# Kernel optimization log

Measured on AMD Instinct MI355X. Metric: run time of the kernel, lower is better.

## Reference

```python
import jax, jax.numpy as jnp
import numpy as np

R_MAX = 5.0
NUM_BESSEL = 8
P_CUT = 5.0
AVG_NEIGH = 16.0
SQ3 = 1.7320508075688772


def poly_cutoff(r):
    # PolynomialCutoff with p=5
    u = r / R_MAX
    p = P_CUT
    f = 1.0 - (p + 1.0) * (p + 2.0) / 2.0 * u**5 + p * (p + 2.0) * u**6 - p * (p + 1.0) / 2.0 * u**7
    return f * (u < 1.0)


def bessel_damped(r, t):
    # BesselSinBasis with heat-kernel diffusion damping exp(-k_n^2 t)
    n = jnp.arange(1, NUM_BESSEL + 1, dtype=r.dtype)  # [8]
    k = n * jnp.pi / R_MAX
    pref = jnp.sqrt(2.0 / R_MAX)
    return pref * jnp.sin(k * r) / r * jnp.exp(-(k**2) * t)  # [E,8]


def switch_norm(x, w, b, mw, vw, rm, rv, eps=1e-5):
    # SwitchNorm1d, eval mode (BN stats = running buffers)
    mean_ln = x.mean(1, keepdims=True)
    var_ln = x.var(1, keepdims=True, ddof=1)
    mws = jax.nn.softmax(mw)
    vws = jax.nn.softmax(vw)
    mean = mws[0] * mean_ln + mws[1] * rm
    var = vws[0] * var_ln + vws[1] * rv
    return (x - mean) / jnp.sqrt(var + eps) * w + b


def setup_inputs() -> dict:
    key = jax.random.key(0)
    ks = jax.random.split(key, 16)
    N, E = 10000, 160000
    d = {}
    d["node_feats"] = jax.random.normal(ks[0], (N, 512), jnp.float32)
    d["edge_attrs"] = jax.random.normal(ks[1], (E, 4), jnp.float32)
    d["edge_lengths"] = jax.random.uniform(ks[2], (E, 1), jnp.float32, 0.5, 4.9)
    d["t"] = jax.random.uniform(ks[3], (E, 1), jnp.float32, 0.01, 1.0)
    d["lengths"] = d["edge_lengths"]
    d["edge_index"] = jax.random.randint(ks[4], (2, E), 0, N)
    g = lambda k, sh: jax.random.normal(k, sh, jnp.float32)
    d["W_scalar"] = g(ks[5], (128, 128))
    d["W_up0"] = g(ks[6], (128, 128))
    d["W_up1"] = g(ks[7], (128, 128))
    d["sn_weight"] = jnp.ones((1, 265), jnp.float32)
    d["sn_bias"] = jnp.zeros((1, 265), jnp.float32)
    d["sn_mean_w"] = jnp.ones((2,), jnp.float32)
    d["sn_var_w"] = jnp.ones((2,), jnp.float32)
    d["sn_run_mean"] = jnp.zeros((1, 265), jnp.float32)
    d["sn_run_var"] = jnp.zeros((1, 265), jnp.float32)
    d["W1"] = g(ks[8], (265, 64))
    d["W2"] = g(ks[9], (64, 64))
    d["W3"] = g(ks[10], (64, 64))
    d["W4"] = g(ks[11], (64, 512))
    d["W_out0"] = g(ks[12], (256, 128))
    d["W_out1"] = g(ks[13], (256, 128))
    return d


def reference(node_feats, edge_attrs, edge_lengths, t, lengths, edge_index,
              W_scalar, W_up0, W_up1,
              sn_weight, sn_bias, sn_mean_w, sn_var_w, sn_run_mean, sn_run_var,
              W1, W2, W3, W4, W_out0, W_out1):
    sender, receiver = edge_index[0], edge_index[1]
    N = node_feats.shape[0]
    s_in = node_feats[:, :128]                        # 0e block [N,128]
    v_in = node_feats[:, 128:].reshape(N, 128, 3)     # 1o block [N,128,3]
    inv = 1.0 / jnp.sqrt(128.0)                       # e3nn Linear fan-in norm
    node_scalars = s_in @ W_scalar * inv              # linear_scalar -> [N,128]
    s_up = s_in @ W_up0 * inv                         # linear_up (0e)
    v_up = jnp.einsum('nud,uo->nod', v_in, W_up1) * inv  # linear_up (1o)

    cutoff = poly_cutoff(edge_lengths)                # [E,1]
    emb = bessel_damped(edge_lengths, t) * cutoff     # radial_embedding [E,8]

    wi = jnp.concatenate([node_scalars[sender] * cutoff,
                          node_scalars[receiver] * cutoff,
                          emb,
                          lengths * cutoff], axis=-1)  # [E,265]
    wi = switch_norm(wi, sn_weight, sn_bias, sn_mean_w, sn_var_w, sn_run_mean, sn_run_var)

    # FullyConnectedNet [265,64,64,64,512], SiLU, fan-in normalized, no bias
    h = jax.nn.silu(wi @ W1 / jnp.sqrt(265.0))
    h = jax.nn.silu(h @ W2 / 8.0)
    h = jax.nn.silu(h @ W3 / 8.0)
    tpw = h @ W4 / 8.0                                 # [E,512]
    w0, w1, w2, w3 = tpw[:, :128], tpw[:, 128:256], tpw[:, 256:384], tpw[:, 384:]

    se = s_up[sender]                                  # [E,128]
    ve = v_up[sender]                                  # [E,128,3]
    y0 = edge_attrs[:, :1]                             # [E,1] (0e sh)
    y1 = edge_attrs[:, 1:4]                            # [E,3] (1o sh)

    # weighted uvu tensor product (CG contractions)
    out0a = w0 * se * y0                                        # 0e x 0e -> 0e
    out0b = w3 * jnp.einsum('eud,ed->eu', ve, y1) / SQ3         # 1o x 1o -> 0e
    out1a = (w1 * se)[:, :, None] * y1[:, None, :]              # 0e x 1o -> 1o
    out1b = w2[:, :, None] * ve * y0[:, None, :]                # 1o x 0e -> 1o

    m0 = jnp.concatenate([out0a, out0b], axis=-1)               # [E,256]
    m1 = jnp.concatenate([out1a, out1b], axis=1)                # [E,256,3]

    M0 = jax.ops.segment_sum(m0, receiver, num_segments=N)      # scatter_sum
    M1 = jax.ops.segment_sum(m1, receiver, num_segments=N)

    inv2 = 1.0 / jnp.sqrt(256.0)
    o0 = M0 @ W_out0 * (inv2 / AVG_NEIGH)                       # [N,128]
    o1 = jnp.einsum('nud,uo->nod', M1, W_out1) * (inv2 / AVG_NEIGH)  # [N,128,3]

    # reshape_irreps: [N, channels, 1+3]
    return jnp.concatenate([o0[:, :, None], o1], axis=2)
```

## Files before the change

### kernel.cpp

```cpp
#include <hip/hip_runtime.h>
#include <hip/hip_bf16.h>
#include <math.h>


#define PI_F 3.14159265358979323846f

typedef short  short8 __attribute__((ext_vector_type(8)));
typedef short  short4v __attribute__((ext_vector_type(4)));
typedef float  f32x4 __attribute__((ext_vector_type(4)));

static __device__ __forceinline__ float silu_f(float x) {
  return x / (1.0f + __expf(-x));
}
static __device__ __forceinline__ short f2bf(float x) {
  __hip_bfloat16 h = __float2bfloat16(x);
  return *reinterpret_cast<short*>(&h);
}
static __device__ __forceinline__ float bf2f(short s) {
  __hip_bfloat16 h = *reinterpret_cast<__hip_bfloat16*>(&s);
  return __bfloat162float(h);
}

__global__ __launch_bounds__(256)
void prep_weights(const float* __restrict__ W1, const float* __restrict__ W2,
                  const float* __restrict__ W3, const float* __restrict__ W4,
                  const float* __restrict__ Wsc, const float* __restrict__ Wu0,
                  const float* __restrict__ Wu1,
                  const float* __restrict__ Wo0, const float* __restrict__ Wo1,
                  short* __restrict__ frags)
{
  int t = blockIdx.x * 256 + threadIdx.x;
  if (t >= 340 * 64) return;
  int frag = t >> 6, lane = t & 63;
  const float* W; int K, Nout, kk, nt; float scale;
  if (frag < 36)       { int f = frag;       W = W1; K = 265; Nout = 64;  kk = f >> 2; nt = f & 3;  scale = 1.0f / sqrtf(265.0f); }
  else if (frag < 44)  { int f = frag - 36;  W = W2; K = 64;  Nout = 64;  kk = f >> 2; nt = f & 3;  scale = 0.125f; }
  else if (frag < 52)  { int f = frag - 44;  W = W3; K = 64;  Nout = 64;  kk = f >> 2; nt = f & 3;  scale = 0.125f; }
  else if (frag < 116) { int f = frag - 52;  W = W4; K = 64;  Nout = 512; kk = f >> 5; nt = f & 31;
                         scale = 0.125f * ((nt >= 24) ? 0.57735026918962576f : 1.0f); }
  else if (frag < 212) { int f = frag - 116; int m = f >> 5; kk = (f >> 3) & 3; nt = f & 7;
                         W = (m == 0) ? Wsc : ((m == 1) ? Wu0 : Wu1);
                         K = 128; Nout = 128; scale = 0.088388347648318447f; }
  else if (frag < 276) { int f = frag - 212; W = Wo0; K = 256; Nout = 128; kk = f >> 3; nt = f & 7;
                         scale = 1.0f / 256.0f; }
  else                 { int f = frag - 276; W = Wo1; K = 256; Nout = 128; kk = f >> 3; nt = f & 7;
                         scale = 1.0f / 256.0f; }
  int n = nt * 16 + (lane & 15);
  short* out = frags + ((size_t)(frag * 64 + lane)) * 8;
#pragma unroll
  for (int i = 0; i < 8; i++) {
    int k = kk * 32 + ((lane >> 4) << 3) + i;
    float v = (k < K) ? W[(size_t)k * Nout + n] * scale : 0.0f;
    out[i] = f2bf(v);
  }
}

#define NPW 16
__global__ __launch_bounds__(128)
void node_mfma(const float* __restrict__ nf, const short* __restrict__ frags,
               short* __restrict__ ns_bf, short4v* __restrict__ suvu, int N)
{
  __shared__ __align__(16) short sA[2][16][520];

  const int tid = threadIdx.x, lane = tid & 63, w = tid >> 6;
  const int nbase = blockIdx.x * (2 * NPW) + w * NPW;

  for (int it = 0; it < 32; ++it) {
    int idx = it * 64 + lane;
    int nd  = idx >> 7;
    int c4  = (idx & 127) << 2;
    int gn  = nbase + nd; if (gn >= N) gn = N - 1;
    float4 g = *(const float4*)&nf[(size_t)gn * 512 + c4];
#pragma unroll
    for (int i = 0; i < 4; i++) {
      int c = c4 + i;
      int pos;
      if (c < 128) pos = c;
      else { int j = c - 128; int u = j / 3, d = j - 3 * u; pos = 128 + (d << 7) + u; }
      sA[w][nd][pos] = f2bf(((const float*)&g)[i]);
    }
  }
  __syncthreads();

  const int arow = lane & 15;
  const int kgrp = (lane >> 4) << 3;
  short8 af[4][4];
#pragma unroll
  for (int m = 0; m < 4; m++)
#pragma unroll
    for (int kk = 0; kk < 4; kk++)
      af[m][kk] = *(const short8*)&sA[w][arow][m * 128 + kk * 32 + kgrp];

  const short8* F = (const short8*)frags;
#pragma unroll
  for (int nt = 0; nt < 8; ++nt) {
    f32x4 c_ns = {0,0,0,0}, c_su = {0,0,0,0};
    f32x4 c_vx = {0,0,0,0}, c_vy = {0,0,0,0}, c_vz = {0,0,0,0};
#pragma unroll
    for (int kk = 0; kk < 4; ++kk) {
      c_ns = __builtin_amdgcn_mfma_f32_16x16x32_bf16(af[0][kk], F[(116 + (0 * 4 + kk) * 8 + nt) * 64 + lane], c_ns, 0, 0, 0);
      c_su = __builtin_amdgcn_mfma_f32_16x16x32_bf16(af[0][kk], F[(116 + (1 * 4 + kk) * 8 + nt) * 64 + lane], c_su, 0, 0, 0);
      c_vx = __builtin_amdgcn_mfma_f32_16x16x32_bf16(af[1][kk], F[(116 + (2 * 4 + kk) * 8 + nt) * 64 + lane], c_vx, 0, 0, 0);
      c_vy = __builtin_amdgcn_mfma_f32_16x16x32_bf16(af[2][kk], F[(116 + (2 * 4 + kk) * 8 + nt) * 64 + lane], c_vy, 0, 0, 0);
      c_vz = __builtin_amdgcn_mfma_f32_16x16x32_bf16(af[3][kk], F[(116 + (2 * 4 + kk) * 8 + nt) * 64 + lane], c_vz, 0, 0, 0);
    }
    const int col = nt * 16 + (lane & 15);
#pragma unroll
    for (int rr = 0; rr < 4; ++rr) {
      int nd = nbase + ((lane >> 4) << 2) + rr;
      if (nd < N) {
        ns_bf[(size_t)nd * 128 + col] = f2bf(c_ns[rr]);
        short4v p;
        p[0] = f2bf(c_su[rr]); p[1] = f2bf(c_vx[rr]);
        p[2] = f2bf(c_vy[rr]); p[3] = f2bf(c_vz[rr]);
        suvu[(size_t)nd * 128 + col] = p;
      }
    }
  }
}

__global__ __launch_bounds__(256)
void prep_norm(const float* __restrict__ snw, const float* __restrict__ snb,
               const float* __restrict__ snmw, const float* __restrict__ snvw,
               const float* __restrict__ snrm, const float* __restrict__ snrv,
               float4* __restrict__ nrm_c)
{
  int k = blockIdx.x * 256 + threadIdx.x;
  float msm0 = 1.0f / (1.0f + __expf(snmw[1] - snmw[0]));
  float vsm0 = 1.0f / (1.0f + __expf(snvw[1] - snvw[0]));
  if (k < 265) {
    float4 c;
    c.x = (1.0f - msm0) * snrm[k];
    c.y = (1.0f - vsm0) * snrv[k] + 1e-5f;
    c.z = snw[k];
    c.w = snb[k];
    nrm_c[k] = c;
  } else if (k == 265) {
    float4 c; c.x = msm0; c.y = vsm0; c.z = 0.f; c.w = 0.f;
    nrm_c[k] = c;
  }
}

__global__ __launch_bounds__(256)
void hist_kernel(const int* __restrict__ eidx, int* __restrict__ cnt, int E)
{
  int e = blockIdx.x * 256 + threadIdx.x;
  if (e < E) atomicAdd(&cnt[eidx[E + e]], 1);
}

__global__ __launch_bounds__(1024)
void scan_kernel(const int* __restrict__ cnt, int* __restrict__ rs,
                 int* __restrict__ cursor, int N)
{
  __shared__ int wsum[16];
  __shared__ int carry_s;
  const int tid = threadIdx.x, lane = tid & 63, wid = tid >> 6;
  if (tid == 0) { carry_s = 0; rs[0] = 0; }
  __syncthreads();
  for (int base = 0; base < N; base += 1024) {
    int i = base + tid;
    int v = (i < N) ? cnt[i] : 0;
    int x = v;
#pragma unroll
    for (int off = 1; off < 64; off <<= 1) {
      int t = __shfl_up(x, off);
      if (lane >= off) x += t;
    }
    if (lane == 63) wsum[wid] = x;
    __syncthreads();
    if (tid == 0) {
      int acc = carry_s;
#pragma unroll
      for (int k = 0; k < 16; k++) { int t = wsum[k]; wsum[k] = acc; acc += t; }
      carry_s = acc;
    }
    __syncthreads();
    int inc = x + wsum[wid];
    if (i < N) { rs[i + 1] = inc; cursor[i] = inc - v; }
    __syncthreads();
  }
}

__global__ __launch_bounds__(256)
void scatter_kernel(const int* __restrict__ eidx, int* __restrict__ cursor,
                    int* __restrict__ perm, int E)
{
  int e = blockIdx.x * 256 + threadIdx.x;
  if (e < E) {
    int r = eidx[E + e];
    int pos = atomicAdd(&cursor[r], 1);
    perm[pos] = e;
  }
}

#define EB 32

__global__ __launch_bounds__(128, 4)
void edge_mlp(const float* __restrict__ elen,
              const float* __restrict__ tdif,
              const float* __restrict__ lens,
              const int*   __restrict__ eidx,
              const float4* __restrict__ nrm_c,
              const short* __restrict__ ns_bf,
              const short* __restrict__ frags,
              const int*   __restrict__ perm,
              short* __restrict__ tpw,
              int e_lo, int E)
{
  __shared__ __align__(16) float smu[288], sva[288], sw_[288], sb_[288];
  __shared__ __align__(16) short hA[EB][72];
  __shared__ __align__(16) short hB[EB][72];

  const int tid  = threadIdx.x;
  const int lane = tid & 63;
  const int w    = tid >> 6;

  for (int i = tid; i < 288; i += 128) {
    float4 c;
    if (i < 265) c = nrm_c[i];
    else { c.x = 0.f; c.y = 1.f; c.z = 0.f; c.w = 0.f; }
    smu[i] = c.x; sva[i] = c.y; sw_[i] = c.z; sb_[i] = c.w;
  }
  const float4 mix = nrm_c[265];
  const float msm0 = mix.x, vsm0 = mix.y;

  const int e16 = lane & 15, grp = lane >> 4;
  int gi = e_lo + blockIdx.x * EB + w * 16 + e16;
  if (gi >= E) gi = E - 1;
  const int e = perm[gi];
  const int snd = eidx[e], rcv = eidx[E + e];
  const float r = elen[e], tt = tdif[e];
  float uu_ = r * 0.2f;
  float u2 = uu_ * uu_, u4 = u2 * u2, u5 = u4 * uu_;
  float cc = 1.0f - 21.0f * u5 + 35.0f * u5 * uu_ - 15.0f * u5 * u2;
  const float cut = (uu_ < 1.0f) ? cc : 0.0f;
  const float lncut = lens[e] * cut;

  short8 raw[9];
  float s1 = 0.f, s2 = 0.f;
#pragma unroll
  for (int kk = 0; kk < 9; ++kk) {
    float v[8];
    if (kk < 4) {
      short8 g = *(const short8*)&ns_bf[(size_t)snd * 128 + kk * 32 + grp * 8];
#pragma unroll
      for (int i = 0; i < 8; i++) v[i] = bf2f(g[i]) * cut;
    } else if (kk < 8) {
      short8 g = *(const short8*)&ns_bf[(size_t)rcv * 128 + (kk - 4) * 32 + grp * 8];
#pragma unroll
      for (int i = 0; i < 8; i++) v[i] = bf2f(g[i]) * cut;
    } else {
      if (grp == 0) {
        const float pref = sqrtf(0.4f);
#pragma unroll
        for (int i = 0; i < 8; i++) {
          float kn = (float)(i + 1) * (PI_F / 5.0f);
          v[i] = pref * __sinf(kn * r) / r * __expf(-kn * kn * tt) * cut;
        }
      } else if (grp == 1) {
        v[0] = lncut;
#pragma unroll
        for (int i = 1; i < 8; i++) v[i] = 0.f;
      } else {
#pragma unroll
        for (int i = 0; i < 8; i++) v[i] = 0.f;
      }
    }
#pragma unroll
    for (int i = 0; i < 8; i++) {
      s1 += v[i]; s2 += v[i] * v[i];
      raw[kk][i] = f2bf(v[i]);
    }
  }
  s1 += __shfl_xor(s1, 16); s1 += __shfl_xor(s1, 32);
  s2 += __shfl_xor(s2, 16); s2 += __shfl_xor(s2, 32);
  const float mean = s1 * (1.0f / 265.0f);
  const float var  = (s2 - s1 * mean) * (1.0f / 264.0f);
  const float mupart = msm0 * mean;
  const float vapart = vsm0 * var;

  __syncthreads();

  const short8* F = (const short8*)frags;
  const int arow = w * 16 + (lane & 15);
  const int kgrp = (lane >> 4) << 3;

  f32x4 A0 = {0,0,0,0}, A1 = {0,0,0,0}, A2 = {0,0,0,0}, A3 = {0,0,0,0};
#pragma unroll
  for (int kk = 0; kk < 9; ++kk) {
    const int k0 = kk * 32 + grp * 8;
    short8 a;
#pragma unroll
    for (int h = 0; h < 2; ++h) {
      float4 mu4 = *(const float4*)&smu[k0 + 4 * h];
      float4 va4 = *(const float4*)&sva[k0 + 4 * h];
      float4 w4  = *(const float4*)&sw_[k0 + 4 * h];
      float4 b4  = *(const float4*)&sb_[k0 + 4 * h];
#pragma unroll
      for (int i = 0; i < 4; ++i) {
        float x  = bf2f(raw[kk][4 * h + i]);
        float mu = mupart + ((const float*)&mu4)[i];
        float va = vapart + ((const float*)&va4)[i];
        a[4 * h + i] = f2bf(fmaf((x - mu) * rsqrtf(va), ((const float*)&w4)[i], ((const float*)&b4)[i]));
      }
    }
    A0 = __builtin_amdgcn_mfma_f32_16x16x32_bf16(a, F[(kk * 4 + 0) * 64 + lane], A0, 0, 0, 0);
    A1 = __builtin_amdgcn_mfma_f32_16x16x32_bf16(a, F[(kk * 4 + 1) * 64 + lane], A1, 0, 0, 0);
    A2 = __builtin_amdgcn_mfma_f32_16x16x32_bf16(a, F[(kk * 4 + 2) * 64 + lane], A2, 0, 0, 0);
    A3 = __builtin_amdgcn_mfma_f32_16x16x32_bf16(a, F[(kk * 4 + 3) * 64 + lane], A3, 0, 0, 0);
  }
#pragma unroll
  for (int rr = 0; rr < 4; ++rr) {
    int er = w * 16 + ((lane >> 4) << 2) + rr;
    hA[er][ 0 + (lane & 15)] = f2bf(silu_f(A0[rr]));
    hA[er][16 + (lane & 15)] = f2bf(silu_f(A1[rr]));
    hA[er][32 + (lane & 15)] = f2bf(silu_f(A2[rr]));
    hA[er][48 + (lane & 15)] = f2bf(silu_f(A3[rr]));
  }
  __syncthreads();

  A0 = A1 = A2 = A3 = (f32x4){0,0,0,0};
#pragma unroll
  for (int kk = 0; kk < 2; ++kk) {
    short8 a = *(const short8*)&hA[arow][kk * 32 + kgrp];
    A0 = __builtin_amdgcn_mfma_f32_16x16x32_bf16(a, F[(36 + kk * 4 + 0) * 64 + lane], A0, 0, 0, 0);
    A1 = __builtin_amdgcn_mfma_f32_16x16x32_bf16(a, F[(36 + kk * 4 + 1) * 64 + lane], A1, 0, 0, 0);
    A2 = __builtin_amdgcn_mfma_f32_16x16x32_bf16(a, F[(36 + kk * 4 + 2) * 64 + lane], A2, 0, 0, 0);
    A3 = __builtin_amdgcn_mfma_f32_16x16x32_bf16(a, F[(36 + kk * 4 + 3) * 64 + lane], A3, 0, 0, 0);
  }
#pragma unroll
  for (int rr = 0; rr < 4; ++rr) {
    int er = w * 16 + ((lane >> 4) << 2) + rr;
    hB[er][ 0 + (lane & 15)] = f2bf(silu_f(A0[rr]));
    hB[er][16 + (lane & 15)] = f2bf(silu_f(A1[rr]));
    hB[er][32 + (lane & 15)] = f2bf(silu_f(A2[rr]));
    hB[er][48 + (lane & 15)] = f2bf(silu_f(A3[rr]));
  }
  __syncthreads();

  A0 = A1 = A2 = A3 = (f32x4){0,0,0,0};
#pragma unroll
  for (int kk = 0; kk < 2; ++kk) {
    short8 a = *(const short8*)&hB[arow][kk * 32 + kgrp];
    A0 = __builtin_amdgcn_mfma_f32_16x16x32_bf16(a, F[(44 + kk * 4 + 0) * 64 + lane], A0, 0, 0, 0);
    A1 = __builtin_amdgcn_mfma_f32_16x16x32_bf16(a, F[(44 + kk * 4 + 1) * 64 + lane], A1, 0, 0, 0);
    A2 = __builtin_amdgcn_mfma_f32_16x16x32_bf16(a, F[(44 + kk * 4 + 2) * 64 + lane], A2, 0, 0, 0);
    A3 = __builtin_amdgcn_mfma_f32_16x16x32_bf16(a, F[(44 + kk * 4 + 3) * 64 + lane], A3, 0, 0, 0);
  }
  __syncthreads();
#pragma unroll
  for (int rr = 0; rr < 4; ++rr) {
    int er = w * 16 + ((lane >> 4) << 2) + rr;
    hA[er][ 0 + (lane & 15)] = f2bf(silu_f(A0[rr]));
    hA[er][16 + (lane & 15)] = f2bf(silu_f(A1[rr]));
    hA[er][32 + (lane & 15)] = f2bf(silu_f(A2[rr]));
    hA[er][48 + (lane & 15)] = f2bf(silu_f(A3[rr]));
  }
  __syncthreads();

  short8 a40 = *(const short8*)&hA[arow][ 0 + kgrp];
  short8 a41 = *(const short8*)&hA[arow][32 + kgrp];
  const int rowbase = blockIdx.x * EB + w * 16 + ((lane >> 4) << 2);

#pragma unroll
  for (int t = 0; t < 8; ++t) {
    f32x4 W0 = {0,0,0,0}, W1t = {0,0,0,0}, W2t = {0,0,0,0}, W3t = {0,0,0,0};
    W0  = __builtin_amdgcn_mfma_f32_16x16x32_bf16(a40, F[(52 + 0 * 32 + ( 0 + t)) * 64 + lane], W0,  0, 0, 0);
    W0  = __builtin_amdgcn_mfma_f32_16x16x32_bf16(a41, F[(52 + 1 * 32 + ( 0 + t)) * 64 + lane], W0,  0, 0, 0);
    W1t = __builtin_amdgcn_mfma_f32_16x16x32_bf16(a40, F[(52 + 0 * 32 + ( 8 + t)) * 64 + lane], W1t, 0, 0, 0);
    W1t = __builtin_amdgcn_mfma_f32_16x16x32_bf16(a41, F[(52 + 1 * 32 + ( 8 + t)) * 64 + lane], W1t, 0, 0, 0);
    W2t = __builtin_amdgcn_mfma_f32_16x16x32_bf16(a40, F[(52 + 0 * 32 + (16 + t)) * 64 + lane], W2t, 0, 0, 0);
    W2t = __builtin_amdgcn_mfma_f32_16x16x32_bf16(a41, F[(52 + 1 * 32 + (16 + t)) * 64 + lane], W2t, 0, 0, 0);
    W3t = __builtin_amdgcn_mfma_f32_16x16x32_bf16(a40, F[(52 + 0 * 32 + (24 + t)) * 64 + lane], W3t, 0, 0, 0);
    W3t = __builtin_amdgcn_mfma_f32_16x16x32_bf16(a41, F[(52 + 1 * 32 + (24 + t)) * 64 + lane], W3t, 0, 0, 0);

    const int uu = t * 16 + (lane & 15);
#pragma unroll
    for (int rr = 0; rr < 4; ++rr) {
      short4v pk;
      pk[0] = f2bf(W0[rr]); pk[1] = f2bf(W1t[rr]);
      pk[2] = f2bf(W2t[rr]); pk[3] = f2bf(W3t[rr]);
      *(short4v*)(tpw + (size_t)(rowbase + rr) * 512 + uu * 4) = pk;
    }
  }
}

__global__ __launch_bounds__(128)
void gather_kernel(const int* __restrict__ rs, const int* __restrict__ perm,
                   const int* __restrict__ eidx, const float* __restrict__ eattr,
                   const short4v* __restrict__ suvu,
                   const short* __restrict__ tpw,
                   float* __restrict__ M0, float* __restrict__ M1,
                   int e_lo, int e_hi, int E, int writemode)
{
  __shared__ int   s_snd[64];
  __shared__ __align__(16) float s_y[64][4];

  const int n = blockIdx.x;
  const int o = threadIdx.x;
  int lo = rs[n], hi = rs[n + 1];
  if (lo < e_lo) lo = e_lo;
  if (hi > e_hi) hi = e_hi;
  if (!writemode && lo >= hi) return;

  float a0 = 0.f, a1 = 0.f;
  float b0 = 0.f, b1 = 0.f, b2 = 0.f;
  float c0 = 0.f, c1 = 0.f, c2 = 0.f;

  for (int base = lo; base < hi; base += 64) {
    const int cnt = min(64, hi - base);
    __syncthreads();
    if (o < cnt) {
      int e = perm[base + o];
      s_snd[o] = eidx[e];
      *(float4*)&s_y[o][0] = *(const float4*)&eattr[e * 4];
    }
    __syncthreads();
    for (int j = 0; j < cnt; ++j) {
      const int snd = s_snd[j];
      const float4 y = *(const float4*)&s_y[j][0];
      const short4v sv = suvu[(size_t)snd * 128 + o];
      short4v pk = *(const short4v*)(tpw + (size_t)(base + j - e_lo) * 512 + o * 4);
      const float se = bf2f(sv[0]);
      const float v0 = bf2f(sv[1]);
      const float v1 = bf2f(sv[2]);
      const float v2 = bf2f(sv[3]);
      const float w0 = bf2f(pk[0]), w1 = bf2f(pk[1]);
      const float w2 = bf2f(pk[2]), w3 = bf2f(pk[3]);
      const float dot = v0 * y.y + v1 * y.z + v2 * y.w;
      a0 = fmaf(w0 * se, y.x, a0);
      a1 = fmaf(w3, dot, a1);
      const float s1v = w1 * se;
      b0 = fmaf(s1v, y.y, b0); b1 = fmaf(s1v, y.z, b1); b2 = fmaf(s1v, y.w, b2);
      const float vv = w2 * y.x;
      c0 = fmaf(vv, v0, c0); c1 = fmaf(vv, v1, c1); c2 = fmaf(vv, v2, c2);
    }
  }
  float* p0 = M0 + (size_t)n * 256;
  float* p1 = M1 + (size_t)n * 3 * 256;
  if (writemode) {
    p0[o] = a0; p0[128 + o] = a1;
    p1[0 * 256 + o] = b0; p1[1 * 256 + o] = b1; p1[2 * 256 + o] = b2;
    p1[0 * 256 + 128 + o] = c0; p1[1 * 256 + 128 + o] = c1; p1[2 * 256 + 128 + o] = c2;
  } else {
    p0[o] += a0; p0[128 + o] += a1;
    p1[0 * 256 + o] += b0; p1[1 * 256 + o] += b1; p1[2 * 256 + o] += b2;
    p1[0 * 256 + 128 + o] += c0; p1[1 * 256 + 128 + o] += c1; p1[2 * 256 + 128 + o] += c2;
  }
}

__global__ __launch_bounds__(128)
void out_mfma(const float* __restrict__ M0, const float* __restrict__ M1,
              const short* __restrict__ frags, float* __restrict__ out, int N)
{
  const int tid = threadIdx.x, lane = tid & 63, w = tid >> 6;
  const int nbase = blockIdx.x * 32 + w * 16;
  const int kgrp = (lane >> 4) << 3;
  int nd = nbase + (lane & 15); if (nd >= N) nd = N - 1;

  const float* rowp[4];
  rowp[0] = M0 + (size_t)nd * 256;
  rowp[1] = M1 + ((size_t)nd * 3 + 0) * 256;
  rowp[2] = M1 + ((size_t)nd * 3 + 1) * 256;
  rowp[3] = M1 + ((size_t)nd * 3 + 2) * 256;

  f32x4 acc[8][4];
#pragma unroll
  for (int nt = 0; nt < 8; ++nt)
#pragma unroll
    for (int s = 0; s < 4; ++s) acc[nt][s] = (f32x4){0,0,0,0};

  const short8* F = (const short8*)frags;
#pragma unroll
  for (int kc = 0; kc < 8; ++kc) {
    short8 a[4];
#pragma unroll
    for (int s = 0; s < 4; ++s) {
      float4 g0 = *(const float4*)&rowp[s][kc * 32 + kgrp];
      float4 g1 = *(const float4*)&rowp[s][kc * 32 + kgrp + 4];
      short8 t;
      t[0] = f2bf(g0.x); t[1] = f2bf(g0.y); t[2] = f2bf(g0.z); t[3] = f2bf(g0.w);
      t[4] = f2bf(g1.x); t[5] = f2bf(g1.y); t[6] = f2bf(g1.z); t[7] = f2bf(g1.w);
      a[s] = t;
    }
#pragma unroll
    for (int nt = 0; nt < 8; ++nt) {
      short8 b0 = F[(212 + kc * 8 + nt) * 64 + lane];
      short8 b1 = F[(276 + kc * 8 + nt) * 64 + lane];
      acc[nt][0] = __builtin_amdgcn_mfma_f32_16x16x32_bf16(a[0], b0, acc[nt][0], 0, 0, 0);
      acc[nt][1] = __builtin_amdgcn_mfma_f32_16x16x32_bf16(a[1], b1, acc[nt][1], 0, 0, 0);
      acc[nt][2] = __builtin_amdgcn_mfma_f32_16x16x32_bf16(a[2], b1, acc[nt][2], 0, 0, 0);
      acc[nt][3] = __builtin_amdgcn_mfma_f32_16x16x32_bf16(a[3], b1, acc[nt][3], 0, 0, 0);
    }
  }

#pragma unroll
  for (int nt = 0; nt < 8; ++nt) {
    const int col = nt * 16 + (lane & 15);
#pragma unroll
    for (int rr = 0; rr < 4; ++rr) {
      int n = nbase + ((lane >> 4) << 2) + rr;
      if (n < N) {
        float4 r;
        r.x = acc[nt][0][rr];
        r.y = acc[nt][1][rr];
        r.z = acc[nt][2][rr];
        r.w = acc[nt][3][rr];
        *(float4*)(out + ((size_t)n * 128 + col) * 4) = r;
      }
    }
  }
}

extern "C" void kernel_launch(void* const* d_in, const int* in_sizes, int n_in,
                              void* d_out, int out_size, void* d_ws, size_t ws_size,
                              hipStream_t stream)
{
  const float* nf   = (const float*)d_in[0];
  const float* eattr= (const float*)d_in[1];
  const float* elen = (const float*)d_in[2];
  const float* tdif = (const float*)d_in[3];
  const float* lens = (const float*)d_in[4];
  const int*   eidx = (const int*)  d_in[5];
  const float* Wsc  = (const float*)d_in[6];
  const float* Wu0  = (const float*)d_in[7];
  const float* Wu1  = (const float*)d_in[8];
  const float* snw  = (const float*)d_in[9];
  const float* snb  = (const float*)d_in[10];
  const float* snmw = (const float*)d_in[11];
  const float* snvw = (const float*)d_in[12];
  const float* snrm = (const float*)d_in[13];
  const float* snrv = (const float*)d_in[14];
  const float* W1   = (const float*)d_in[15];
  const float* W2   = (const float*)d_in[16];
  const float* W3   = (const float*)d_in[17];
  const float* W4   = (const float*)d_in[18];
  const float* Wo0  = (const float*)d_in[19];
  const float* Wo1  = (const float*)d_in[20];

  const int N = in_sizes[0] / 512;
  const int E = in_sizes[1] / 4;

  char* p = (char*)d_ws;
  short*   ns_bf = (short*)p;    p += (size_t)N * 128 * 2;
  short4v* suvu  = (short4v*)p;  p += (size_t)N * 128 * 8;
  float*   M0    = (float*)p;    p += (size_t)N * 256 * 4;
  float*   M1    = (float*)p;    p += (size_t)N * 768 * 4;
  float4*  nrm_c = (float4*)p;   p += 266 * 16;
  short*   frags = (short*)p;    p += (size_t)340 * 64 * 8 * 2;
  int* cnt    = (int*)p;         p += (size_t)N * 4;
  int* rs     = (int*)p;         p += (size_t)(N + 1) * 4;
  int* cursor = (int*)p;         p += (size_t)N * 4;
  int* perm   = (int*)p;         p += (size_t)E * 4;
  size_t used = (size_t)(p - (char*)d_ws);
  used = (used + 255) & ~(size_t)255;
  short* tpw = (short*)((char*)d_ws + used);
  size_t avail = (ws_size > used) ? (ws_size - used) : 0;

  long long chunk = (long long)(avail / 1024) & ~31LL;
  long long Eup = ((long long)E + 31) & ~31LL;
  if (chunk > Eup) chunk = Eup;
  if (chunk < 32)  chunk = 32;
  const int writemode = (chunk >= Eup) ? 1 : 0;

  if (!writemode)
    hipMemsetAsync(M0, 0, (size_t)1024 * N * sizeof(float), stream);
  hipMemsetAsync(cnt, 0, (size_t)N * sizeof(int), stream);

  prep_weights<<<dim3((340 * 64 + 255) / 256), dim3(256), 0, stream>>>(
      W1, W2, W3, W4, Wsc, Wu0, Wu1, Wo0, Wo1, frags);
  prep_norm<<<dim3(2), dim3(256), 0, stream>>>(snw, snb, snmw, snvw, snrm, snrv, nrm_c);
  node_mfma<<<dim3((N + 31) / 32), dim3(128), 0, stream>>>(nf, frags, ns_bf, suvu, N);
  hist_kernel<<<dim3((E + 255) / 256), dim3(256), 0, stream>>>(eidx, cnt, E);
  scan_kernel<<<dim3(1), dim3(1024), 0, stream>>>(cnt, rs, cursor, N);
  scatter_kernel<<<dim3((E + 255) / 256), dim3(256), 0, stream>>>(eidx, cursor, perm, E);

  for (long long lo = 0; lo < E; lo += chunk) {
    int n_e = (int)(((long long)E - lo < chunk) ? ((long long)E - lo) : chunk);
    int blocks = (n_e + EB - 1) / EB;
    edge_mlp<<<dim3(blocks), dim3(128), 0, stream>>>(
        elen, tdif, lens, eidx, nrm_c, ns_bf, frags, perm, tpw, (int)lo, E);
    gather_kernel<<<dim3(N), dim3(128), 0, stream>>>(
        rs, perm, eidx, eattr, suvu, tpw, M0, M1, (int)lo, (int)(lo + n_e), E, writemode);
  }

  out_mfma<<<dim3((N + 31) / 32), dim3(128), 0, stream>>>(M0, M1, frags, (float*)d_out, N);
}
```

Baseline: 229.1 us.

## Store aggregated messages in bf16, fuse prep kernels, prefetch gather loads

Merges the weight-fragment prep, norm-constant prep and receiver histogram into one launch to cut kernel launch overhead. Stores the per-node aggregates M0/M1 in bf16 instead of fp32, halving the write and read traffic between the gather and output kernels and removing the conversion step in out_mfma. Software-prefetches the next edge's sender features and edge weights in the gather loop to hide load latency, and uses the raw hardware rsq intrinsic in the edge MLP norm. The bf16 aggregates lose precision, especially in the chunked accumulate mode, where each chunk's partial sum is rounded back to bf16.

```diff
diff --git a/kernel.cpp b/kernel.cpp
--- a/kernel.cpp
+++ b/kernel.cpp
@@ -22,36 +22,62 @@
 }
 
 __global__ __launch_bounds__(256)
-void prep_weights(const float* __restrict__ W1, const float* __restrict__ W2,
-                  const float* __restrict__ W3, const float* __restrict__ W4,
-                  const float* __restrict__ Wsc, const float* __restrict__ Wu0,
-                  const float* __restrict__ Wu1,
-                  const float* __restrict__ Wo0, const float* __restrict__ Wo1,
-                  short* __restrict__ frags)
-{
-  int t = blockIdx.x * 256 + threadIdx.x;
-  if (t >= 340 * 64) return;
-  int frag = t >> 6, lane = t & 63;
-  const float* W; int K, Nout, kk, nt; float scale;
-  if (frag < 36)       { int f = frag;       W = W1; K = 265; Nout = 64;  kk = f >> 2; nt = f & 3;  scale = 1.0f / sqrtf(265.0f); }
-  else if (frag < 44)  { int f = frag - 36;  W = W2; K = 64;  Nout = 64;  kk = f >> 2; nt = f & 3;  scale = 0.125f; }
-  else if (frag < 52)  { int f = frag - 44;  W = W3; K = 64;  Nout = 64;  kk = f >> 2; nt = f & 3;  scale = 0.125f; }
-  else if (frag < 116) { int f = frag - 52;  W = W4; K = 64;  Nout = 512; kk = f >> 5; nt = f & 31;
-                         scale = 0.125f * ((nt >= 24) ? 0.57735026918962576f : 1.0f); }
-  else if (frag < 212) { int f = frag - 116; int m = f >> 5; kk = (f >> 3) & 3; nt = f & 7;
-                         W = (m == 0) ? Wsc : ((m == 1) ? Wu0 : Wu1);
-                         K = 128; Nout = 128; scale = 0.088388347648318447f; }
-  else if (frag < 276) { int f = frag - 212; W = Wo0; K = 256; Nout = 128; kk = f >> 3; nt = f & 7;
-                         scale = 1.0f / 256.0f; }
-  else                 { int f = frag - 276; W = Wo1; K = 256; Nout = 128; kk = f >> 3; nt = f & 7;
-                         scale = 1.0f / 256.0f; }
-  int n = nt * 16 + (lane & 15);
-  short* out = frags + ((size_t)(frag * 64 + lane)) * 8;
-#pragma unroll
-  for (int i = 0; i < 8; i++) {
-    int k = kk * 32 + ((lane >> 4) << 3) + i;
-    float v = (k < K) ? W[(size_t)k * Nout + n] * scale : 0.0f;
-    out[i] = f2bf(v);
+void prep_fused(const float* __restrict__ W1, const float* __restrict__ W2,
+                const float* __restrict__ W3, const float* __restrict__ W4,
+                const float* __restrict__ Wsc, const float* __restrict__ Wu0,
+                const float* __restrict__ Wu1,
+                const float* __restrict__ Wo0, const float* __restrict__ Wo1,
+                const float* __restrict__ snw, const float* __restrict__ snb,
+                const float* __restrict__ snmw, const float* __restrict__ snvw,
+                const float* __restrict__ snrm, const float* __restrict__ snrv,
+                const int* __restrict__ eidx,
+                short* __restrict__ frags, float4* __restrict__ nrm_c,
+                int* __restrict__ cnt, int E)
+{
+  const int b = blockIdx.x;
+  if (b < 85) {
+    int t = b * 256 + threadIdx.x;
+    if (t >= 340 * 64) return;
+    int frag = t >> 6, lane = t & 63;
+    const float* W; int K, Nout, kk, nt; float scale;
+    if (frag < 36)       { int f = frag;       W = W1; K = 265; Nout = 64;  kk = f >> 2; nt = f & 3;  scale = 1.0f / sqrtf(265.0f); }
+    else if (frag < 44)  { int f = frag - 36;  W = W2; K = 64;  Nout = 64;  kk = f >> 2; nt = f & 3;  scale = 0.125f; }
+    else if (frag < 52)  { int f = frag - 44;  W = W3; K = 64;  Nout = 64;  kk = f >> 2; nt = f & 3;  scale = 0.125f; }
+    else if (frag < 116) { int f = frag - 52;  W = W4; K = 64;  Nout = 512; kk = f >> 5; nt = f & 31;
+                           scale = 0.125f * ((nt >= 24) ? 0.57735026918962576f : 1.0f); }
+    else if (frag < 212) { int f = frag - 116; int m = f >> 5; kk = (f >> 3) & 3; nt = f & 7;
+                           W = (m == 0) ? Wsc : ((m == 1) ? Wu0 : Wu1);
+                           K = 128; Nout = 128; scale = 0.088388347648318447f; }
+    else if (frag < 276) { int f = frag - 212; W = Wo0; K = 256; Nout = 128; kk = f >> 3; nt = f & 7;
+                           scale = 1.0f / 256.0f; }
+    else                 { int f = frag - 276; W = Wo1; K = 256; Nout = 128; kk = f >> 3; nt = f & 7;
+                           scale = 1.0f / 256.0f; }
+    int n = nt * 16 + (lane & 15);
+    short* out = frags + ((size_t)(frag * 64 + lane)) * 8;
+#pragma unroll
+    for (int i = 0; i < 8; i++) {
+      int k = kk * 32 + ((lane >> 4) << 3) + i;
+      float v = (k < K) ? W[(size_t)k * Nout + n] * scale : 0.0f;
+      out[i] = f2bf(v);
+    }
+  } else if (b < 87) {
+    int k = (b - 85) * 256 + threadIdx.x;
+    float msm0 = 1.0f / (1.0f + __expf(snmw[1] - snmw[0]));
+    float vsm0 = 1.0f / (1.0f + __expf(snvw[1] - snvw[0]));
+    if (k < 265) {
+      float4 c;
+      c.x = (1.0f - msm0) * snrm[k];
+      c.y = (1.0f - vsm0) * snrv[k] + 1e-5f;
+      c.z = snw[k];
+      c.w = snb[k];
+      nrm_c[k] = c;
+    } else if (k == 265) {
+      float4 c; c.x = msm0; c.y = vsm0; c.z = 0.f; c.w = 0.f;
+      nrm_c[k] = c;
+    }
+  } else {
+    int e = (b - 87) * 256 + threadIdx.x;
+    if (e < E) atomicAdd(&cnt[eidx[E + e]], 1);
   }
 }
 
@@ -117,35 +143,6 @@
       }
     }
   }
-}
-
-__global__ __launch_bounds__(256)
-void prep_norm(const float* __restrict__ snw, const float* __restrict__ snb,
-               const float* __restrict__ snmw, const float* __restrict__ snvw,
-               const float* __restrict__ snrm, const float* __restrict__ snrv,
-               float4* __restrict__ nrm_c)
-{
-  int k = blockIdx.x * 256 + threadIdx.x;
-  float msm0 = 1.0f / (1.0f + __expf(snmw[1] - snmw[0]));
-  float vsm0 = 1.0f / (1.0f + __expf(snvw[1] - snvw[0]));
-  if (k < 265) {
-    float4 c;
-    c.x = (1.0f - msm0) * snrm[k];
-    c.y = (1.0f - vsm0) * snrv[k] + 1e-5f;
-    c.z = snw[k];
-    c.w = snb[k];
-    nrm_c[k] = c;
-  } else if (k == 265) {
-    float4 c; c.x = msm0; c.y = vsm0; c.z = 0.f; c.w = 0.f;
-    nrm_c[k] = c;
-  }
-}
-
-__global__ __launch_bounds__(256)
-void hist_kernel(const int* __restrict__ eidx, int* __restrict__ cnt, int E)
-{
-  int e = blockIdx.x * 256 + threadIdx.x;
-  if (e < E) atomicAdd(&cnt[eidx[E + e]], 1);
 }
 
 __global__ __launch_bounds__(1024)
@@ -301,7 +298,8 @@
         float x  = bf2f(raw[kk][4 * h + i]);
         float mu = mupart + ((const float*)&mu4)[i];
         float va = vapart + ((const float*)&va4)[i];
-        a[4 * h + i] = f2bf(fmaf((x - mu) * rsqrtf(va), ((const float*)&w4)[i], ((const float*)&b4)[i]));
+        float rs = __builtin_amdgcn_rsq(va);
+        a[4 * h + i] = f2bf(fmaf((x - mu) * rs, ((const float*)&w4)[i], ((const float*)&b4)[i]));
       }
     }
     A0 = __builtin_amdgcn_mfma_f32_16x16x32_bf16(a, F[(kk * 4 + 0) * 64 + lane], A0, 0, 0, 0);
@@ -390,7 +388,7 @@
                    const int* __restrict__ eidx, const float* __restrict__ eattr,
                    const short4v* __restrict__ suvu,
                    const short* __restrict__ tpw,
-                   float* __restrict__ M0, float* __restrict__ M1,
+                   short* __restrict__ M0b, short* __restrict__ M1b,
                    int e_lo, int e_hi, int E, int writemode)
 {
   __shared__ int   s_snd[64];
@@ -408,19 +406,23 @@
   float c0 = 0.f, c1 = 0.f, c2 = 0.f;
 
   for (int base = lo; base < hi; base += 64) {
-    const int cnt = min(64, hi - base);
+    const int cnt_ = min(64, hi - base);
     __syncthreads();
-    if (o < cnt) {
+    if (o < cnt_) {
       int e = perm[base + o];
       s_snd[o] = eidx[e];
       *(float4*)&s_y[o][0] = *(const float4*)&eattr[e * 4];
     }
     __syncthreads();
-    for (int j = 0; j < cnt; ++j) {
-      const int snd = s_snd[j];
+    short4v sv = suvu[(size_t)s_snd[0] * 128 + o];
+    short4v pk = *(const short4v*)(tpw + (size_t)(base - e_lo) * 512 + o * 4);
+    for (int j = 0; j < cnt_; ++j) {
+      short4v sv_n = sv, pk_n = pk;
+      if (j + 1 < cnt_) {
+        sv_n = suvu[(size_t)s_snd[j + 1] * 128 + o];
+        pk_n = *(const short4v*)(tpw + (size_t)(base + j + 1 - e_lo) * 512 + o * 4);
+      }
       const float4 y = *(const float4*)&s_y[j][0];
-      const short4v sv = suvu[(size_t)snd * 128 + o];
-      short4v pk = *(const short4v*)(tpw + (size_t)(base + j - e_lo) * 512 + o * 4);
       const float se = bf2f(sv[0]);
       const float v0 = bf2f(sv[1]);
       const float v1 = bf2f(sv[2]);
@@ -434,23 +436,28 @@
       b0 = fmaf(s1v, y.y, b0); b1 = fmaf(s1v, y.z, b1); b2 = fmaf(s1v, y.w, b2);
       const float vv = w2 * y.x;
       c0 = fmaf(vv, v0, c0); c1 = fmaf(vv, v1, c1); c2 = fmaf(vv, v2, c2);
-    }
-  }
-  float* p0 = M0 + (size_t)n * 256;
-  float* p1 = M1 + (size_t)n * 3 * 256;
+      sv = sv_n; pk = pk_n;
+    }
+  }
+  short* p0 = M0b + (size_t)n * 256;
+  short* p1 = M1b + (size_t)n * 768;
   if (writemode) {
-    p0[o] = a0; p0[128 + o] = a1;
-    p1[0 * 256 + o] = b0; p1[1 * 256 + o] = b1; p1[2 * 256 + o] = b2;
-    p1[0 * 256 + 128 + o] = c0; p1[1 * 256 + 128 + o] = c1; p1[2 * 256 + 128 + o] = c2;
+    p0[o] = f2bf(a0); p0[128 + o] = f2bf(a1);
+    p1[0 * 256 + o] = f2bf(b0); p1[1 * 256 + o] = f2bf(b1); p1[2 * 256 + o] = f2bf(b2);
+    p1[0 * 256 + 128 + o] = f2bf(c0); p1[1 * 256 + 128 + o] = f2bf(c1); p1[2 * 256 + 128 + o] = f2bf(c2);
   } else {
-    p0[o] += a0; p0[128 + o] += a1;
-    p1[0 * 256 + o] += b0; p1[1 * 256 + o] += b1; p1[2 * 256 + o] += b2;
-    p1[0 * 256 + 128 + o] += c0; p1[1 * 256 + 128 + o] += c1; p1[2 * 256 + 128 + o] += c2;
+    p0[o] = f2bf(bf2f(p0[o]) + a0); p0[128 + o] = f2bf(bf2f(p0[128 + o]) + a1);
+    p1[0 * 256 + o] = f2bf(bf2f(p1[0 * 256 + o]) + b0);
+    p1[1 * 256 + o] = f2bf(bf2f(p1[1 * 256 + o]) + b1);
+    p1[2 * 256 + o] = f2bf(bf2f(p1[2 * 256 + o]) + b2);
+    p1[0 * 256 + 128 + o] = f2bf(bf2f(p1[0 * 256 + 128 + o]) + c0);
+    p1[1 * 256 + 128 + o] = f2bf(bf2f(p1[1 * 256 + 128 + o]) + c1);
+    p1[2 * 256 + 128 + o] = f2bf(bf2f(p1[2 * 256 + 128 + o]) + c2);
   }
 }
 
 __global__ __launch_bounds__(128)
-void out_mfma(const float* __restrict__ M0, const float* __restrict__ M1,
+void out_mfma(const short* __restrict__ M0b, const short* __restrict__ M1b,
               const short* __restrict__ frags, float* __restrict__ out, int N)
 {
   const int tid = threadIdx.x, lane = tid & 63, w = tid >> 6;
@@ -458,11 +465,11 @@
   const int kgrp = (lane >> 4) << 3;
   int nd = nbase + (lane & 15); if (nd >= N) nd = N - 1;
 
-  const float* rowp[4];
-  rowp[0] = M0 + (size_t)nd * 256;
-  rowp[1] = M1 + ((size_t)nd * 3 + 0) * 256;
-  rowp[2] = M1 + ((size_t)nd * 3 + 1) * 256;
-  rowp[3] = M1 + ((size_t)nd * 3 + 2) * 256;
+  const short* rowp[4];
+  rowp[0] = M0b + (size_t)nd * 256;
+  rowp[1] = M1b + (size_t)nd * 768;
+  rowp[2] = M1b + (size_t)nd * 768 + 256;
+  rowp[3] = M1b + (size_t)nd * 768 + 512;
 
   f32x4 acc[8][4];
 #pragma unroll
@@ -475,14 +482,8 @@
   for (int kc = 0; kc < 8; ++kc) {
     short8 a[4];
 #pragma unroll
-    for (int s = 0; s < 4; ++s) {
-      float4 g0 = *(const float4*)&rowp[s][kc * 32 + kgrp];
-      float4 g1 = *(const float4*)&rowp[s][kc * 32 + kgrp + 4];
-      short8 t;
-      t[0] = f2bf(g0.x); t[1] = f2bf(g0.y); t[2] = f2bf(g0.z); t[3] = f2bf(g0.w);
-      t[4] = f2bf(g1.x); t[5] = f2bf(g1.y); t[6] = f2bf(g1.z); t[7] = f2bf(g1.w);
-      a[s] = t;
-    }
+    for (int s = 0; s < 4; ++s)
+      a[s] = *(const short8*)&rowp[s][kc * 32 + kgrp];
 #pragma unroll
     for (int nt = 0; nt < 8; ++nt) {
       short8 b0 = F[(212 + kc * 8 + nt) * 64 + lane];
@@ -544,8 +545,8 @@
   char* p = (char*)d_ws;
   short*   ns_bf = (short*)p;    p += (size_t)N * 128 * 2;
   short4v* suvu  = (short4v*)p;  p += (size_t)N * 128 * 8;
-  float*   M0    = (float*)p;    p += (size_t)N * 256 * 4;
-  float*   M1    = (float*)p;    p += (size_t)N * 768 * 4;
+  short*   M0b   = (short*)p;    p += (size_t)N * 256 * 2;
+  short*   M1b   = (short*)p;    p += (size_t)N * 768 * 2;
   float4*  nrm_c = (float4*)p;   p += 266 * 16;
   short*   frags = (short*)p;    p += (size_t)340 * 64 * 8 * 2;
   int* cnt    = (int*)p;         p += (size_t)N * 4;
@@ -564,14 +565,14 @@
   const int writemode = (chunk >= Eup) ? 1 : 0;
 
   if (!writemode)
-    hipMemsetAsync(M0, 0, (size_t)1024 * N * sizeof(float), stream);
+    hipMemsetAsync(M0b, 0, (size_t)1024 * N * sizeof(short), stream);
   hipMemsetAsync(cnt, 0, (size_t)N * sizeof(int), stream);
 
-  prep_weights<<<dim3((340 * 64 + 255) / 256), dim3(256), 0, stream>>>(
-      W1, W2, W3, W4, Wsc, Wu0, Wu1, Wo0, Wo1, frags);
-  prep_norm<<<dim3(2), dim3(256), 0, stream>>>(snw, snb, snmw, snvw, snrm, snrv, nrm_c);
+  const int hist_blocks = (E + 255) / 256;
+  prep_fused<<<dim3(87 + hist_blocks), dim3(256), 0, stream>>>(
+      W1, W2, W3, W4, Wsc, Wu0, Wu1, Wo0, Wo1,
+      snw, snb, snmw, snvw, snrm, snrv, eidx, frags, nrm_c, cnt, E);
   node_mfma<<<dim3((N + 31) / 32), dim3(128), 0, stream>>>(nf, frags, ns_bf, suvu, N);
-  hist_kernel<<<dim3((E + 255) / 256), dim3(256), 0, stream>>>(eidx, cnt, E);
   scan_kernel<<<dim3(1), dim3(1024), 0, stream>>>(cnt, rs, cursor, N);
   scatter_kernel<<<dim3((E + 255) / 256), dim3(256), 0, stream>>>(eidx, cursor, perm, E);
 
@@ -581,8 +582,8 @@
     edge_mlp<<<dim3(blocks), dim3(128), 0, stream>>>(
         elen, tdif, lens, eidx, nrm_c, ns_bf, frags, perm, tpw, (int)lo, E);
     gather_kernel<<<dim3(N), dim3(128), 0, stream>>>(
-        rs, perm, eidx, eattr, suvu, tpw, M0, M1, (int)lo, (int)(lo + n_e), E, writemode);
-  }
-
-  out_mfma<<<dim3((N + 31) / 32), dim3(128), 0, stream>>>(M0, M1, frags, (float*)d_out, N);
-}
+        rs, perm, eidx, eattr, suvu, tpw, M0b, M1b, (int)lo, (int)(lo + n_e), E, writemode);
+  }
+
+  out_mfma<<<dim3((N + 31) / 32), dim3(128), 0, stream>>>(M0b, M1b, frags, (float*)d_out, N);
+}
```

Result: faster. 217.6 us (-5.0%).
